# Kernel tuning notes

Measured on AMD Instinct MI355X. Metric: run time of the kernel, lower is better.

## Reference

```python
import jax, jax.numpy as jnp
import numpy as np

B, S, D = 2, 1024, 2048
H, KVH, HD = 16, 4, 128
HID, E, K = 4096, 8, 2
EPS = 1e-5
NEG = -1e9  # finite stand-in for -inf in the causal mask


def setup_inputs() -> dict:
    key = jax.random.key(0)
    ks = jax.random.split(key, 16)
    sc = 0.02
    x = jax.random.normal(ks[0], (B, S, D), jnp.float32)
    # rotary tables (theta = 10000), as cos/sin instead of complex
    inv_freq = 1.0 / (10000.0 ** (jnp.arange(0, HD, 2, dtype=jnp.float32) / HD))
    t = jnp.arange(S, dtype=jnp.float32)
    fr = jnp.outer(t, inv_freq)  # [S, HD/2]
    freqs_cos, freqs_sin = jnp.cos(fr), jnp.sin(fr)
    positions = jnp.arange(S, dtype=jnp.int32)
    mask = jnp.where(jnp.tril(jnp.ones((S, S), bool)), 0.0, NEG).astype(jnp.float32)
    attn_norm_w = jnp.ones((D,), jnp.float32)
    ffn_norm_w = jnp.ones((D,), jnp.float32)
    wq = jax.random.normal(ks[1], (D, H * HD), jnp.float32) * sc
    wk = jax.random.normal(ks[2], (D, KVH * HD), jnp.float32) * sc
    wv = jax.random.normal(ks[3], (D, KVH * HD), jnp.float32) * sc
    wo = jax.random.normal(ks[4], (H * HD, D), jnp.float32) * sc
    gate_w = jax.random.normal(ks[5], (D, E), jnp.float32) * sc
    w1 = jax.random.normal(ks[6], (E, D, HID), jnp.float32) * sc
    w2 = jax.random.normal(ks[7], (E, HID, D), jnp.float32) * sc
    w3 = jax.random.normal(ks[8], (E, D, HID), jnp.float32) * sc
    return dict(x=x, freqs_cos=freqs_cos, freqs_sin=freqs_sin, positions=positions,
                mask=mask, attn_norm_w=attn_norm_w, ffn_norm_w=ffn_norm_w,
                wq=wq, wk=wk, wv=wv, wo=wo, gate_w=gate_w, w1=w1, w2=w2, w3=w3)


def rmsnorm(x, w):
    xf = x.astype(jnp.float32)
    n = xf * jax.lax.rsqrt(jnp.mean(xf * xf, axis=-1, keepdims=True) + EPS)
    return n.astype(x.dtype) * w


def rope(t, cos, sin):
    # t: [B,S,nh,HD]; interleaved (real, imag) pairs like torch.view_as_complex
    tr = t.reshape(*t.shape[:-1], HD // 2, 2)
    xr, xi = tr[..., 0], tr[..., 1]
    c = cos[None, :, None, :]
    s = sin[None, :, None, :]
    out = jnp.stack([xr * c - xi * s, xr * s + xi * c], axis=-1)
    return out.reshape(t.shape)


def block_fwd(x, freqs_cos, freqs_sin, mask, attn_norm_w, ffn_norm_w,
              wq, wk, wv, wo, gate_w, w1, w2, w3):
    # ---- attention ----
    h = rmsnorm(x, attn_norm_w)
    q = (h @ wq).reshape(B, S, H, HD)
    k = (h @ wk).reshape(B, S, KVH, HD)
    v = (h @ wv).reshape(B, S, KVH, HD)
    q = rope(q, freqs_cos, freqs_sin)
    k = rope(k, freqs_cos, freqs_sin)
    rep = H // KVH
    k = jnp.repeat(k, rep, axis=2)  # [B,S,H,HD]
    v = jnp.repeat(v, rep, axis=2)
    scale = HD ** -0.5
    scores = jnp.einsum('bqhd,bkhd->bhqk', q, k) * scale + mask[None, None]
    probs = jax.nn.softmax(scores.astype(jnp.float32), axis=-1).astype(q.dtype)
    attn = jnp.einsum('bhqk,bkhd->bqhd', probs, v).reshape(B, S, H * HD)
    h1 = x + attn @ wo
    # ---- MoE FFN ----
    t = rmsnorm(h1, ffn_norm_w).reshape(-1, D)  # [T,D]
    logits = t @ gate_w  # [T,E]
    topw, sel = jax.lax.top_k(logits, K)
    topw = jax.nn.softmax(topw.astype(jnp.float32), axis=-1).astype(t.dtype)
    out = jnp.zeros_like(t)
    for i in range(E):
        coef = jnp.sum(jnp.where(sel == i, topw, 0.0), axis=-1, keepdims=True)  # [T,1]
        ff = (jax.nn.silu(t @ w1[i]) * (t @ w3[i])) @ w2[i]
        out = out + coef * ff
    return h1 + out.reshape(B, S, D)


def reference(x, freqs_cos, freqs_sin, positions, mask, attn_norm_w, ffn_norm_w,
              wq, wk, wv, wo, gate_w, w1, w2, w3):
    # prefill branch (positions.shape[0] > 1): KV-cache scatter is a write-only
    # side effect in the original and does not affect this output.
    del positions
    return block_fwd(x, freqs_cos, freqs_sin, mask, attn_norm_w, ffn_norm_w,
                     wq, wk, wv, wo, gate_w, w1, w2, w3)
```

## Files before the change

kernel.cpp:

```cpp
#include <hip/hip_runtime.h>

typedef unsigned short u16;
typedef unsigned int u32;
typedef __bf16 bf16x8 __attribute__((ext_vector_type(8)));
typedef _Float16 f16;
typedef f16 f16x8 __attribute__((ext_vector_type(8)));
typedef float f32x4 __attribute__((ext_vector_type(4)));
typedef u32 u32x2 __attribute__((ext_vector_type(2)));

#define DEVFN __device__ __forceinline__

constexpr int kB = 2, kS = 1024, kD = 2048, kH = 16, kKVH = 4, kHD = 128;
constexpr int kHID = 4096, kE = 8;
constexpr int kRows = kB * kS;
constexpr int kQKVN = kH*kHD + 2*kKVH*kHD;
constexpr int kSlotsPad = 5120;
constexpr int kMaxTiles = 40;
constexpr float kEps = 1e-5f;
constexpr float kNeg = -1000000000.0f;
constexpr float kScale = 0.08838834764831845f;

DEVFN u16 f2bf(float f) {
  u32 u = __float_as_uint(f);
  return (u16)((u + 0x7fffu + ((u >> 16) & 1u)) >> 16);
}
DEVFN float bf2f(u16 u) { u32 v = ((u32)u) << 16; return __uint_as_float(v); }

DEVFN void split8v(float4 a, float4 b, f16x8& hi, f16x8& lo) {
  float v[8] = {a.x, a.y, a.z, a.w, b.x, b.y, b.z, b.w};
  #pragma unroll
  for (int e = 0; e < 8; ++e) {
    f16 h = (f16)v[e];
    hi[e] = h;
    lo[e] = (f16)(v[e] - (float)h);
  }
}

DEVFN void gll16(const void* g, void* l) {
  __builtin_amdgcn_global_load_lds(
      (const __attribute__((address_space(1))) void*)g,
      (__attribute__((address_space(3))) void*)l, 16, 0, 0);
}

DEVFN u32x2 pk4bf(float a, float b, float c, float d) {
  union { __bf16 h[4]; u32x2 w; } u;
  u.h[0] = (__bf16)a; u.h[1] = (__bf16)b;
  u.h[2] = (__bf16)c; u.h[3] = (__bf16)d;
  return u.w;
}

__global__ __launch_bounds__(256) void rms_split_kernel(const float* __restrict__ in,
    const float* __restrict__ w, f16* __restrict__ oh, f16* __restrict__ ol) {
  int row = blockIdx.x, tid = threadIdx.x;
  const float* x = in + (size_t)row * kD;
  float4 v0 = *(const float4*)&x[tid*8];
  float4 v1 = *(const float4*)&x[tid*8+4];
  float ss = v0.x*v0.x+v0.y*v0.y+v0.z*v0.z+v0.w*v0.w
           + v1.x*v1.x+v1.y*v1.y+v1.z*v1.z+v1.w*v1.w;
  #pragma unroll
  for (int off = 32; off; off >>= 1) ss += __shfl_xor(ss, off);
  __shared__ float red[4];
  if ((tid & 63) == 0) red[tid >> 6] = ss;
  __syncthreads();
  float tot = red[0] + red[1] + red[2] + red[3];
  float rs = rsqrtf(tot * (1.0f/kD) + kEps);
  float4 w0 = *(const float4*)&w[tid*8];
  float4 w1 = *(const float4*)&w[tid*8+4];
  float4 o0, o1;
  o0.x = v0.x*rs*w0.x; o0.y = v0.y*rs*w0.y; o0.z = v0.z*rs*w0.z; o0.w = v0.w*rs*w0.w;
  o1.x = v1.x*rs*w1.x; o1.y = v1.y*rs*w1.y; o1.z = v1.z*rs*w1.z; o1.w = v1.w*rs*w1.w;
  f16x8 hi, lo;
  split8v(o0, o1, hi, lo);
  *(f16x8*)&oh[(size_t)row*kD + tid*8] = hi;
  *(f16x8*)&ol[(size_t)row*kD + tid*8] = lo;
}

__global__ __launch_bounds__(256) void rms_bf16_kernel(const float* __restrict__ in,
    const float* __restrict__ w, u16* __restrict__ out) {
  int row = blockIdx.x, tid = threadIdx.x;
  const float* x = in + (size_t)row * kD;
  float4 v0 = *(const float4*)&x[tid*8];
  float4 v1 = *(const float4*)&x[tid*8+4];
  float ss = v0.x*v0.x+v0.y*v0.y+v0.z*v0.z+v0.w*v0.w
           + v1.x*v1.x+v1.y*v1.y+v1.z*v1.z+v1.w*v1.w;
  #pragma unroll
  for (int off = 32; off; off >>= 1) ss += __shfl_xor(ss, off);
  __shared__ float red[4];
  if ((tid & 63) == 0) red[tid >> 6] = ss;
  __syncthreads();
  float tot = red[0] + red[1] + red[2] + red[3];
  float rs = rsqrtf(tot * (1.0f/kD) + kEps);
  float4 w0 = *(const float4*)&w[tid*8];
  float4 w1 = *(const float4*)&w[tid*8+4];
  union { int4 i4; u16 u[8]; } pk;
  pk.u[0] = f2bf(v0.x*rs*w0.x); pk.u[1] = f2bf(v0.y*rs*w0.y);
  pk.u[2] = f2bf(v0.z*rs*w0.z); pk.u[3] = f2bf(v0.w*rs*w0.w);
  pk.u[4] = f2bf(v1.x*rs*w1.x); pk.u[5] = f2bf(v1.y*rs*w1.y);
  pk.u[6] = f2bf(v1.z*rs*w1.z); pk.u[7] = f2bf(v1.w*rs*w1.w);
  *(int4*)&out[(size_t)row*kD + tid*8] = pk.i4;
}

__global__ void transpose_split_kernel(const float* __restrict__ in,
    f16* __restrict__ hi, f16* __restrict__ lo, int R, int C, int noff, int ldout) {
  __shared__ float tile[32][33];
  int c0 = blockIdx.x * 32, r0 = blockIdx.y * 32;
  int tx = threadIdx.x, ty = threadIdx.y;
  #pragma unroll
  for (int i = 0; i < 32; i += 8)
    tile[ty + i][tx] = in[(size_t)(r0 + ty + i) * C + c0 + tx];
  __syncthreads();
  #pragma unroll
  for (int i = 0; i < 32; i += 8) {
    float v = tile[tx][ty + i];
    f16 h = (f16)v;
    size_t o = (size_t)(noff + c0 + ty + i) * ldout + r0 + tx;
    hi[o] = h;
    lo[o] = (f16)(v - (float)h);
  }
}

__global__ void vt_split_kernel(const float* __restrict__ qkv,
    f16* __restrict__ vTh, f16* __restrict__ vTl) {
  __shared__ float tile[32][33];
  int s0 = blockIdx.x * 32, c0 = blockIdx.y * 32, b = blockIdx.z;
  int tx = threadIdx.x, ty = threadIdx.y;
  #pragma unroll
  for (int i = 0; i < 32; i += 8)
    tile[ty + i][tx] = qkv[(size_t)(b*kS + s0 + ty + i) * kQKVN + kH*kHD + kKVH*kHD + c0 + tx];
  __syncthreads();
  #pragma unroll
  for (int i = 0; i < 32; i += 8) {
    float v = tile[tx][ty + i];
    f16 h = (f16)v;
    size_t o = (size_t)(b*kKVH*kHD + c0 + ty + i) * kS + s0 + tx;
    vTh[o] = h;
    vTl[o] = (f16)(v - (float)h);
  }
}

template<bool ADDX>
__global__ __launch_bounds__(256) void gemm_sf16_kernel(
    const f16* __restrict__ Ah0, const f16* __restrict__ Al0, int lda,
    const f16* __restrict__ Bh0, const f16* __restrict__ Bl0,
    float* __restrict__ C, int ldc, int coff,
    const float* __restrict__ X, int ldx, int K) {
  __shared__ __align__(16) u16 Ah[128*64], Al[128*64], Bh[128*64], Bl[128*64];
  int tid = threadIdx.x, lane = tid & 63, w = tid >> 6;
  int bm = blockIdx.y * 128, bn = blockIdx.x * 128;
  int wr = w >> 1, wc = w & 1;
  int hg = lane >> 4, lid = lane & 15;
  f32x4 acc[4][4] = {};
  const f16 *aH[4], *aL[4], *bH[4], *bL[4];
  #pragma unroll
  for (int j = 0; j < 4; ++j) {
    int r = w*32 + j*8 + (lane >> 3);
    int colc = ((lane & 7) ^ (r & 7)) * 8;
    aH[j] = Ah0 + (size_t)(bm + r) * lda + colc;
    aL[j] = Al0 + (size_t)(bm + r) * lda + colc;
    bH[j] = Bh0 + (size_t)(bn + r) * K + colc;
    bL[j] = Bl0 + (size_t)(bn + r) * K + colc;
  }
  const char* AhB = (const char*)Ah; const char* AlB = (const char*)Al;
  const char* BhB = (const char*)Bh; const char* BlB = (const char*)Bl;
  for (int kt = 0; kt < K; kt += 64) {
    __syncthreads();
    #pragma unroll
    for (int j = 0; j < 4; ++j) {
      int lb = w*2048 + j*512;
      gll16(aH[j] + kt, &Ah[lb]);
      gll16(aL[j] + kt, &Al[lb]);
      gll16(bH[j] + kt, &Bh[lb]);
      gll16(bL[j] + kt, &Bl[lb]);
    }
    __syncthreads();
    #pragma unroll
    for (int kk = 0; kk < 2; ++kk) {
      f16x8 ah[4], al[4], bh[4], bl[4];
      #pragma unroll
      for (int f = 0; f < 4; ++f) {
        int rA = wr*64 + f*16 + lid;
        int oA = (rA*128 + kk*64 + hg*16) ^ ((rA & 7) << 4);
        ah[f] = *(const f16x8*)(AhB + oA);
        al[f] = *(const f16x8*)(AlB + oA);
        int rB = wc*64 + f*16 + lid;
        int oB = (rB*128 + kk*64 + hg*16) ^ ((rB & 7) << 4);
        bh[f] = *(const f16x8*)(BhB + oB);
        bl[f] = *(const f16x8*)(BlB + oB);
      }
      __builtin_amdgcn_s_setprio(1);
      #pragma unroll
      for (int i = 0; i < 4; ++i)
        #pragma unroll
        for (int j = 0; j < 4; ++j) {
          acc[i][j] = __builtin_amdgcn_mfma_f32_16x16x32_f16(ah[i], bh[j], acc[i][j], 0, 0, 0);
          acc[i][j] = __builtin_amdgcn_mfma_f32_16x16x32_f16(ah[i], bl[j], acc[i][j], 0, 0, 0);
          acc[i][j] = __builtin_amdgcn_mfma_f32_16x16x32_f16(al[i], bh[j], acc[i][j], 0, 0, 0);
        }
      __builtin_amdgcn_s_setprio(0);
    }
  }
  #pragma unroll
  for (int i = 0; i < 4; ++i) {
    #pragma unroll
    for (int rr = 0; rr < 4; ++rr) {
      size_t gr = (size_t)(bm + wr*64 + i*16 + hg*4 + rr);
      #pragma unroll
      for (int j = 0; j < 4; ++j) {
        int gc = bn + wc*64 + j*16 + lid;
        float v = acc[i][j][rr];
        if (ADDX) v += X[gr * ldx + gc];
        C[gr * ldc + coff + gc] = v;
      }
    }
  }
}

__global__ __launch_bounds__(256) void rope_kernel(float* __restrict__ qkv,
    const float* __restrict__ fc, const float* __restrict__ fs,
    f16* __restrict__ Kh, f16* __restrict__ Kl) {
  int idx = blockIdx.x * 256 + threadIdx.x;
  constexpr int NQ = kB*kS*kH*(kHD/2);
  constexpr int NK = kB*kS*kKVH*(kHD/2);
  if (idx < NQ) {
    int i = idx & 63, h = (idx >> 6) & 15, s = (idx >> 10) & 1023, b = idx >> 20;
    size_t base = ((size_t)(b*kS + s))*kQKVN + h*kHD + 2*i;
    float c = fc[s*64 + i], sn = fs[s*64 + i];
    float xr = qkv[base], xi = qkv[base+1];
    qkv[base]   = xr*c - xi*sn;
    qkv[base+1] = xr*sn + xi*c;
  } else {
    int j = idx - NQ; if (j >= NK) return;
    int i = j & 63, h = (j >> 6) & 3, s = (j >> 8) & 1023, b = j >> 18;
    size_t src = ((size_t)(b*kS + s))*kQKVN + kH*kHD + h*kHD + 2*i;
    float c = fc[s*64 + i], sn = fs[s*64 + i];
    float xr = qkv[src], xi = qkv[src+1];
    float o0 = xr*c - xi*sn, o1 = xr*sn + xi*c;
    size_t dst = (((size_t)(b*kKVH + h))*kS + s)*kHD + 2*i;
    f16 h0 = (f16)o0, h1 = (f16)o1;
    Kh[dst]   = h0; Kl[dst]   = (f16)(o0 - (float)h0);
    Kh[dst+1] = h1; Kl[dst+1] = (f16)(o1 - (float)h1);
  }
}

__global__ __launch_bounds__(256) void attn_sf16_kernel(const float* __restrict__ qkv,
    const f16* __restrict__ Ksh, const f16* __restrict__ Ksl,
    const f16* __restrict__ vTh, const f16* __restrict__ vTl,
    f16* __restrict__ outh, f16* __restrict__ outl) {
  int qt = (int)gridDim.x - 1 - blockIdx.x;
  int h = blockIdx.y, b = blockIdx.z;
  int kvh = h >> 2;
  int q0 = qt * 64;
  __shared__ __align__(16) char Kh[64*128*2], Kl[64*128*2];
  __shared__ __align__(16) char Vh[128*64*2], Vl[128*64*2];
  __shared__ __align__(16) char Ph[4][16*64*2], Pl[4][16*64*2];
  int tid = threadIdx.x, lane = tid & 63, w = tid >> 6;
  int hg = lane >> 4, lid = lane & 15;

  f16x8 qh[4], ql[4];
  {
    const float* qrow = qkv + (size_t)(b*kS + q0 + w*16 + lid) * kQKVN + h*kHD;
    #pragma unroll
    for (int ks = 0; ks < 4; ++ks) {
      float4 a = *(const float4*)(qrow + ks*32 + hg*8);
      float4 c = *(const float4*)(qrow + ks*32 + hg*8 + 4);
      split8v(a, c, qh[ks], ql[ks]);
    }
  }
  f32x4 oacc[8] = {};
  float m[4] = {-3.0e38f, -3.0e38f, -3.0e38f, -3.0e38f};
  float lsum[4] = {};
  char* Phw = Ph[w];
  char* Plw = Pl[w];

  for (int kt = 0; kt <= qt; ++kt) {
    __syncthreads();
    {
      int r = tid >> 2, c0 = (tid & 3) * 32;
      const f16* khr = Ksh + ((size_t)(b*kKVH + kvh)*kS + kt*64 + r) * kHD + c0;
      const f16* klr = Ksl + ((size_t)(b*kKVH + kvh)*kS + kt*64 + r) * kHD + c0;
      #pragma unroll
      for (int s8 = 0; s8 < 4; ++s8) {
        int4 hi = *(const int4*)(khr + s8*8);
        int4 lo = *(const int4*)(klr + s8*8);
        int off = (r*256 + c0*2 + s8*16) ^ ((r & 7) << 4);
        *(int4*)(Kh + off) = hi;
        *(int4*)(Kl + off) = lo;
      }
    }
    {
      int r = tid >> 1, c0 = (tid & 1) * 32;
      const f16* vhr = vTh + (size_t)(b*kKVH*kHD + kvh*kHD + r) * kS + kt*64 + c0;
      const f16* vlr = vTl + (size_t)(b*kKVH*kHD + kvh*kHD + r) * kS + kt*64 + c0;
      #pragma unroll
      for (int s8 = 0; s8 < 4; ++s8) {
        int4 hi = *(const int4*)(vhr + s8*8);
        int4 lo = *(const int4*)(vlr + s8*8);
        int off = (r*128 + c0*2 + s8*16) ^ ((r & 7) << 4);
        *(int4*)(Vh + off) = hi;
        *(int4*)(Vl + off) = lo;
      }
    }
    __syncthreads();

    f32x4 sacc[4] = {};
    __builtin_amdgcn_s_setprio(1);
    #pragma unroll
    for (int ks = 0; ks < 4; ++ks) {
      #pragma unroll
      for (int j = 0; j < 4; ++j) {
        int rB = j*16 + lid;
        int off = (rB*256 + ks*64 + hg*16) ^ ((rB & 7) << 4);
        f16x8 kh = *(const f16x8*)(Kh + off);
        f16x8 klo = *(const f16x8*)(Kl + off);
        sacc[j] = __builtin_amdgcn_mfma_f32_16x16x32_f16(qh[ks], kh, sacc[j], 0, 0, 0);
        sacc[j] = __builtin_amdgcn_mfma_f32_16x16x32_f16(qh[ks], klo, sacc[j], 0, 0, 0);
        sacc[j] = __builtin_amdgcn_mfma_f32_16x16x32_f16(ql[ks], kh, sacc[j], 0, 0, 0);
      }
    }
    __builtin_amdgcn_s_setprio(0);
    float s[4][4], ps[4][4];
    bool diag = (kt == qt);
    #pragma unroll
    for (int j = 0; j < 4; ++j)
      #pragma unroll
      for (int r = 0; r < 4; ++r) {
        float v = sacc[j][r] * kScale;
        if (diag) {
          int kvabs = kt*64 + j*16 + lid;
          int qabs = q0 + w*16 + hg*4 + r;
          if (kvabs > qabs) v = kNeg;
        }
        s[j][r] = v;
      }
    float pm[4], cf[4];
    #pragma unroll
    for (int r = 0; r < 4; ++r) {
      pm[r] = fmaxf(fmaxf(s[0][r], s[1][r]), fmaxf(s[2][r], s[3][r]));
      #pragma unroll
      for (int msk = 1; msk < 16; msk <<= 1) pm[r] = fmaxf(pm[r], __shfl_xor(pm[r], msk));
      float mn = fmaxf(m[r], pm[r]);
      cf[r] = __expf(m[r] - mn);
      m[r] = mn;
    }
    #pragma unroll
    for (int j2 = 0; j2 < 8; ++j2)
      #pragma unroll
      for (int r = 0; r < 4; ++r) oacc[j2][r] *= cf[r];
    float rs[4] = {};
    #pragma unroll
    for (int j = 0; j < 4; ++j)
      #pragma unroll
      for (int r = 0; r < 4; ++r) {
        float p = __expf(s[j][r] - m[r]);
        ps[j][r] = p;
        rs[r] += p;
      }
    #pragma unroll
    for (int r = 0; r < 4; ++r) lsum[r] = lsum[r]*cf[r] + rs[r];
    #pragma unroll
    for (int j = 0; j < 4; ++j)
      #pragma unroll
      for (int r = 0; r < 4; ++r) {
        int q = hg*4 + r;
        int off = (q*128 + (j*16 + lid)*2) ^ ((q & 7) << 4);
        f16 ph = (f16)ps[j][r];
        *(f16*)(Phw + off) = ph;
        *(f16*)(Plw + off) = (f16)(ps[j][r] - (float)ph);
      }
    #pragma unroll
    for (int kk2 = 0; kk2 < 2; ++kk2) {
      int oP = (lid*128 + kk2*64 + hg*16) ^ ((lid & 7) << 4);
      f16x8 pa_h = *(const f16x8*)(Phw + oP);
      f16x8 pa_l = *(const f16x8*)(Plw + oP);
      __builtin_amdgcn_s_setprio(1);
      #pragma unroll
      for (int j2 = 0; j2 < 8; ++j2) {
        int rV = j2*16 + lid;
        int off = (rV*128 + kk2*64 + hg*16) ^ ((rV & 7) << 4);
        f16x8 vh = *(const f16x8*)(Vh + off);
        f16x8 vl = *(const f16x8*)(Vl + off);
        oacc[j2] = __builtin_amdgcn_mfma_f32_16x16x32_f16(pa_h, vh, oacc[j2], 0, 0, 0);
        oacc[j2] = __builtin_amdgcn_mfma_f32_16x16x32_f16(pa_h, vl, oacc[j2], 0, 0, 0);
        oacc[j2] = __builtin_amdgcn_mfma_f32_16x16x32_f16(pa_l, vh, oacc[j2], 0, 0, 0);
      }
      __builtin_amdgcn_s_setprio(0);
    }
  }
  #pragma unroll
  for (int r = 0; r < 4; ++r) {
    #pragma unroll
    for (int msk = 1; msk < 16; msk <<= 1) lsum[r] += __shfl_xor(lsum[r], msk);
    lsum[r] = 1.f / lsum[r];
  }
  #pragma unroll
  for (int j2 = 0; j2 < 8; ++j2)
    #pragma unroll
    for (int r = 0; r < 4; ++r) {
      size_t o = (size_t)(b*kS + q0 + w*16 + hg*4 + r) * kD + h*kHD + j2*16 + lid;
      float v = oacc[j2][r] * lsum[r];
      f16 hh = (f16)v;
      outh[o] = hh;
      outl[o] = (f16)(v - (float)hh);
    }
}

__global__ void zero_counts_kernel(int* counts) {
  if (threadIdx.x < kE) counts[threadIdx.x] = 0;
}

__global__ __launch_bounds__(64) void gate_kernel(const float* __restrict__ h1,
    const float* __restrict__ wn, const float* __restrict__ gw,
    int* __restrict__ packA, int* __restrict__ packB,
    float* __restrict__ cA, float* __restrict__ cB,
    int* __restrict__ lists, int* __restrict__ counts) {
  int row = blockIdx.x, lane = threadIdx.x;
  const float* x = h1 + (size_t)row * kD;
  float ss = 0.f;
  for (int d = lane; d < kD; d += 64) { float v = x[d]; ss = fmaf(v, v, ss); }
  #pragma unroll
  for (int off = 32; off; off >>= 1) ss += __shfl_xor(ss, off);
  float rs = rsqrtf(ss * (1.0f/kD) + kEps);
  float acc[kE] = {};
  for (int d = lane; d < kD; d += 64) {
    float g = x[d] * rs * wn[d];
    const float* gr = gw + (size_t)d * kE;
    #pragma unroll
    for (int e = 0; e < kE; ++e) acc[e] = fmaf(g, gr[e], acc[e]);
  }
  #pragma unroll
  for (int e = 0; e < kE; ++e)
    #pragma unroll
    for (int off = 32; off; off >>= 1) acc[e] += __shfl_xor(acc[e], off);
  if (lane == 0) {
    int i1 = 0; float l1 = acc[0];
    #pragma unroll
    for (int e = 1; e < kE; ++e) if (acc[e] > l1) { l1 = acc[e]; i1 = e; }
    int i2 = -1; float l2 = -3.4e38f;
    #pragma unroll
    for (int e = 0; e < kE; ++e) if (e != i1 && acc[e] > l2) { l2 = acc[e]; i2 = e; }
    float e2 = __expf(l2 - l1);
    float inv = 1.f / (1.f + e2);
    int p1 = atomicAdd(&counts[i1], 1); lists[i1*kRows + p1] = row;
    int p2 = atomicAdd(&counts[i2], 1); lists[i2*kRows + p2] = row;
    packA[row] = i1*2048 + p1; cA[row] = inv;
    packB[row] = i2*2048 + p2; cB[row] = e2 * inv;
  }
}

__global__ void prefix_kernel(const int* __restrict__ counts,
    int* __restrict__ padbase, int* __restrict__ tileTab) {
  if (threadIdx.x == 0) {
    int base = 0, idx = 0;
    for (int e = 0; e < kE; ++e) {
      padbase[e] = base;
      int nt = (counts[e] + 127) >> 7;
      for (int t = 0; t < nt; ++t) tileTab[idx++] = (e << 8) | t;
      base += nt << 7;
    }
    for (; idx < kMaxTiles; ++idx) tileTab[idx] = -1;
  }
}

__global__ __launch_bounds__(512, 4) void gemm_up_kernel(
    const u16* __restrict__ A, const float* __restrict__ W1, const float* __restrict__ W3,
    u16* __restrict__ hid, const int* __restrict__ lists,
    const int* __restrict__ counts, const int* __restrict__ padbase,
    const int* __restrict__ tileTab) {
  int tab = tileTab[blockIdx.y];
  if (tab < 0) return;
  int e = tab >> 8, mb = tab & 255;
  int cnt = counts[e];
  int bm = mb * 128;
  int slot0 = padbase[e] + bm;
  const int* ids = lists + e * kRows;
  int g = blockIdx.x;
  __shared__ __align__(16) char SM[65536];
  u16* As[2]   = { (u16*)SM, (u16*)(SM + 16384) };
  char* B1s[2] = { SM + 32768, SM + 40960 };
  char* B3s[2] = { SM + 49152, SM + 57344 };
  int tid = threadIdx.x, lane = tid & 63, w = tid >> 6;
  int wr = w >> 2, wcc = w & 3;
  int hg = lane >> 4, lid = lane & 15;
  f32x4 acc[4][2] = {};

  const u16* aP[2];
  #pragma unroll
  for (int j = 0; j < 2; ++j) {
    int r = w*16 + j*8 + (lane >> 3);
    int colc = ((lane & 7) ^ (r & 7)) * 8;
    int rr = bm + r; if (rr >= cnt) rr = cnt - 1;
    aP[j] = A + (size_t)ids[rr] * kD + colc;
  }
  const float* b1e = W1 + (size_t)e*kD*kHID + (size_t)g*64 + lane;
  const float* b3e = W3 + (size_t)e*kD*kHID + (size_t)g*64 + lane;
  int wOff[2];
  #pragma unroll
  for (int s = 0; s < 2; ++s)
    wOff[s] = (lane*128 + w*16 + s*8) ^ ((lane & 7) << 4);

  auto stageA = [&](int buf, int t) {
    int kt = t * 64;
    #pragma unroll
    for (int j = 0; j < 2; ++j) gll16(aP[j] + kt, &As[buf][w*1024 + j*512]);
  };
  float r1v[2][4], r3v[2][4];
  auto loadB = [&](int t) {
    int kt = t * 64;
    #pragma unroll
    for (int s = 0; s < 2; ++s)
      #pragma unroll
      for (int j = 0; j < 4; ++j) {
        size_t ko = (size_t)(kt + w*8 + s*4 + j) * kHID;
        r1v[s][j] = b1e[ko];
        r3v[s][j] = b3e[ko];
      }
  };
  auto writeB = [&](int buf) {
    #pragma unroll
    for (int s = 0; s < 2; ++s) {
      *(u32x2*)(B1s[buf] + wOff[s]) = pk4bf(r1v[s][0], r1v[s][1], r1v[s][2], r1v[s][3]);
      *(u32x2*)(B3s[buf] + wOff[s]) = pk4bf(r3v[s][0], r3v[s][1], r3v[s][2], r3v[s][3]);
    }
  };
  auto compute = [&](int buf) {
    const char* AsB = (const char*)As[buf];
    const char* Bb = (wcc >= 2) ? B3s[buf] : B1s[buf];
    #pragma unroll
    for (int kk = 0; kk < 2; ++kk) {
      bf16x8 af[4], bfv[2];
      #pragma unroll
      for (int f = 0; f < 4; ++f) {
        int rA = wr*64 + f*16 + lid;
        af[f] = *(const bf16x8*)(AsB + ((rA*128 + kk*64 + hg*16) ^ ((rA & 7) << 4)));
      }
      #pragma unroll
      for (int f = 0; f < 2; ++f) {
        int rB = (wcc & 1)*32 + f*16 + lid;
        bfv[f] = *(const bf16x8*)(Bb + ((rB*128 + kk*64 + hg*16) ^ ((rB & 7) << 4)));
      }
      __builtin_amdgcn_s_setprio(1);
      #pragma unroll
      for (int i = 0; i < 4; ++i)
        #pragma unroll
        for (int j = 0; j < 2; ++j)
          acc[i][j] = __builtin_amdgcn_mfma_f32_16x16x32_bf16(af[i], bfv[j], acc[i][j], 0, 0, 0);
      __builtin_amdgcn_s_setprio(0);
    }
  };

  constexpr int NT = kD / 64;
  stageA(0, 0);
  loadB(0);
  writeB(0);
  __syncthreads();
  for (int t = 0; t < NT; t += 2) {
    stageA(1, t+1); loadB(t+1);
    compute(0);
    writeB(1);
    __syncthreads();
    if (t+2 < NT) { stageA(0, t+2); loadB(t+2); }
    compute(1);
    if (t+2 < NT) writeB(0);
    __syncthreads();
  }

  float* Xch = (float*)SM;
  if (wcc < 2) {
    #pragma unroll
    for (int i = 0; i < 4; ++i)
      #pragma unroll
      for (int rr = 0; rr < 4; ++rr) {
        int row = wr*64 + i*16 + hg*4 + rr;
        #pragma unroll
        for (int j = 0; j < 2; ++j)
          Xch[row*64 + (wcc & 1)*32 + j*16 + lid] = acc[i][j][rr];
      }
  }
  __syncthreads();
  if (wcc >= 2) {
    #pragma unroll
    for (int i = 0; i < 4; ++i)
      #pragma unroll
      for (int rr = 0; rr < 4; ++rr) {
        int row = wr*64 + i*16 + hg*4 + rr;
        int gr = bm + row;
        if (gr >= cnt) continue;
        u16* orow = hid + (size_t)(slot0 + row) * kHID + g*64 + (wcc & 1)*32;
        #pragma unroll
        for (int j = 0; j < 2; ++j) {
          int col = j*16 + lid;
          float g1 = Xch[row*64 + (wcc & 1)*32 + col];
          float g3 = acc[i][j][rr];
          orow[col] = f2bf(g1 / (1.f + __expf(-g1)) * g3);
        }
      }
  }
}

__global__ __launch_bounds__(512, 4) void gemm_down_kernel(
    const u16* __restrict__ hid, const float* __restrict__ W2,
    u16* __restrict__ ff, const int* __restrict__ padbase,
    const int* __restrict__ tileTab) {
  int tab = tileTab[blockIdx.y];
  if (tab < 0) return;
  int e = tab >> 8, mb = tab & 255;
  int slot0 = padbase[e] + mb * 128;
  int bn = blockIdx.x * 128;
  __shared__ __align__(16) char SM[65536];
  u16* As[2] = { (u16*)SM, (u16*)(SM + 16384) };
  char* Bs[2] = { SM + 32768, SM + 49152 };
  int tid = threadIdx.x, lane = tid & 63, w = tid >> 6;
  int wr = w >> 2, wc = w & 3;
  int hg = lane >> 4, lid = lane & 15;
  f32x4 acc[4][2] = {};

  const u16* aP[2];
  #pragma unroll
  for (int j = 0; j < 2; ++j) {
    int r = w*16 + j*8 + (lane >> 3);
    int colc = ((lane & 7) ^ (r & 7)) * 8;
    aP[j] = hid + (size_t)(slot0 + r) * kHID + colc;
  }
  int nrow = tid & 127;
  int kq = tid >> 7;
  const float* b2e = W2 + (size_t)e*kHID*kD + (size_t)bn + nrow;
  int wOff[4];
  #pragma unroll
  for (int s = 0; s < 4; ++s)
    wOff[s] = (nrow*128 + kq*32 + s*8) ^ ((nrow & 7) << 4);

  auto stageA = [&](int buf, int t) {
    int kt = t * 64;
    #pragma unroll
    for (int j = 0; j < 2; ++j) gll16(aP[j] + kt, &As[buf][w*1024 + j*512]);
  };
  float rbv[4][4];
  auto loadB = [&](int t) {
    int kt = t * 64;
    #pragma unroll
    for (int s = 0; s < 4; ++s)
      #pragma unroll
      for (int j = 0; j < 4; ++j)
        rbv[s][j] = b2e[(size_t)(kt + kq*16 + s*4 + j) * kD];
  };
  auto writeB = [&](int buf) {
    #pragma unroll
    for (int s = 0; s < 4; ++s)
      *(u32x2*)(Bs[buf] + wOff[s]) = pk4bf(rbv[s][0], rbv[s][1], rbv[s][2], rbv[s][3]);
  };
  auto compute = [&](int buf) {
    const char* AsB = (const char*)As[buf];
    const char* Bb = Bs[buf];
    #pragma unroll
    for (int kk = 0; kk < 2; ++kk) {
      bf16x8 af[4], bfv[2];
      #pragma unroll
      for (int f = 0; f < 4; ++f) {
        int rA = wr*64 + f*16 + lid;
        af[f] = *(const bf16x8*)(AsB + ((rA*128 + kk*64 + hg*16) ^ ((rA & 7) << 4)));
      }
      #pragma unroll
      for (int f = 0; f < 2; ++f) {
        int rB = wc*32 + f*16 + lid;
        bfv[f] = *(const bf16x8*)(Bb + ((rB*128 + kk*64 + hg*16) ^ ((rB & 7) << 4)));
      }
      __builtin_amdgcn_s_setprio(1);
      #pragma unroll
      for (int i = 0; i < 4; ++i)
        #pragma unroll
        for (int j = 0; j < 2; ++j)
          acc[i][j] = __builtin_amdgcn_mfma_f32_16x16x32_bf16(af[i], bfv[j], acc[i][j], 0, 0, 0);
      __builtin_amdgcn_s_setprio(0);
    }
  };

  constexpr int NT = kHID / 64;
  stageA(0, 0);
  loadB(0);
  writeB(0);
  __syncthreads();
  for (int t = 0; t < NT; t += 2) {
    stageA(1, t+1); loadB(t+1);
    compute(0);
    writeB(1);
    __syncthreads();
    if (t+2 < NT) { stageA(0, t+2); loadB(t+2); }
    compute(1);
    if (t+2 < NT) writeB(0);
    __syncthreads();
  }

  #pragma unroll
  for (int i = 0; i < 4; ++i)
    #pragma unroll
    for (int rr = 0; rr < 4; ++rr) {
      int row = wr*64 + i*16 + hg*4 + rr;
      u16* orow = ff + (size_t)(slot0 + row) * kD + bn;
      #pragma unroll
      for (int j = 0; j < 2; ++j)
        orow[wc*32 + j*16 + lid] = f2bf(acc[i][j][rr]);
    }
}

__global__ __launch_bounds__(256) void moe_combine_kernel(
    const u16* __restrict__ ff, const int* __restrict__ padbase,
    const int* __restrict__ packA, const int* __restrict__ packB,
    const float* __restrict__ cA, const float* __restrict__ cB,
    float* __restrict__ outp) {
  int row = blockIdx.x, tid = threadIdx.x;
  int pa = packA[row], pb = packB[row];
  int sa = padbase[pa >> 11] + (pa & 2047);
  int sb = padbase[pb >> 11] + (pb & 2047);
  float ca = cA[row], cb = cB[row];
  union { int4 i4; u16 u[8]; } va, vb;
  va.i4 = *(const int4*)(ff + (size_t)sa * kD + tid*8);
  vb.i4 = *(const int4*)(ff + (size_t)sb * kD + tid*8);
  float* o = outp + (size_t)row * kD + tid*8;
  float4 o0 = *(const float4*)o;
  float4 o1 = *(const float4*)(o + 4);
  o0.x += ca*bf2f(va.u[0]) + cb*bf2f(vb.u[0]);
  o0.y += ca*bf2f(va.u[1]) + cb*bf2f(vb.u[1]);
  o0.z += ca*bf2f(va.u[2]) + cb*bf2f(vb.u[2]);
  o0.w += ca*bf2f(va.u[3]) + cb*bf2f(vb.u[3]);
  o1.x += ca*bf2f(va.u[4]) + cb*bf2f(vb.u[4]);
  o1.y += ca*bf2f(va.u[5]) + cb*bf2f(vb.u[5]);
  o1.z += ca*bf2f(va.u[6]) + cb*bf2f(vb.u[6]);
  o1.w += ca*bf2f(va.u[7]) + cb*bf2f(vb.u[7]);
  *(float4*)o = o0;
  *(float4*)(o + 4) = o1;
}

extern "C" void kernel_launch(void* const* d_in, const int* in_sizes, int n_in,
                              void* d_out, int out_size, void* d_ws, size_t ws_size,
                              hipStream_t stream) {
  const float* x    = (const float*)d_in[0];
  const float* fcos = (const float*)d_in[1];
  const float* fsin = (const float*)d_in[2];
  const float* anw  = (const float*)d_in[5];
  const float* fnw  = (const float*)d_in[6];
  const float* wq   = (const float*)d_in[7];
  const float* wk   = (const float*)d_in[8];
  const float* wv   = (const float*)d_in[9];
  const float* wo   = (const float*)d_in[10];
  const float* gw   = (const float*)d_in[11];
  const float* w1   = (const float*)d_in[12];
  const float* w2   = (const float*)d_in[13];
  const float* w3   = (const float*)d_in[14];
  float* outp = (float*)d_out;

  char* ws = (char*)d_ws;
  size_t off = 0;
  auto alloc = [&](size_t bytes) -> void* {
    void* p = ws + off; off += (bytes + 255) & ~(size_t)255; return p;
  };
  f16* h16h   = (f16*)alloc((size_t)kRows*kD*2);
  f16* h16l   = (f16*)alloc((size_t)kRows*kD*2);
  float* qkv  = (float*)alloc((size_t)kRows*kQKVN*4);
  f16* Ksh    = (f16*)alloc((size_t)kB*kKVH*kS*kHD*2);
  f16* Ksl    = (f16*)alloc((size_t)kB*kKVH*kS*kHD*2);
  f16* vTh    = (f16*)alloc((size_t)kB*kKVH*kHD*kS*2);
  f16* vTl    = (f16*)alloc((size_t)kB*kKVH*kHD*kS*2);
  f16* a16h   = (f16*)alloc((size_t)kRows*kD*2);
  f16* a16l   = (f16*)alloc((size_t)kRows*kD*2);
  u16* tbf    = (u16*)alloc((size_t)kRows*kD*2);
  int* packA  = (int*)alloc(kRows*4);
  int* packB  = (int*)alloc(kRows*4);
  float* cAv  = (float*)alloc(kRows*4);
  float* cBv  = (float*)alloc(kRows*4);
  int* counts = (int*)alloc(kE*4);
  int* padbase= (int*)alloc(kE*4);
  int* tileTab= (int*)alloc(kMaxTiles*4);
  int* lists  = (int*)alloc((size_t)kE*kRows*4);
  f16* Bqh    = (f16*)alloc((size_t)kQKVN*kD*2);
  f16* Bql    = (f16*)alloc((size_t)kQKVN*kD*2);
  f16* Bwh    = (f16*)alloc((size_t)kD*kD*2);
  f16* Bwl    = (f16*)alloc((size_t)kD*kD*2);
  u16* hid    = (u16*)alloc((size_t)kSlotsPad*kHID*2);
  u16* ffb    = (u16*)alloc((size_t)kSlotsPad*kD*2);

  transpose_split_kernel<<<dim3(kD/32, kD/32), dim3(32,8), 0, stream>>>(wq, Bqh, Bql, kD, 2048, 0, kD);
  transpose_split_kernel<<<dim3(512/32, kD/32), dim3(32,8), 0, stream>>>(wk, Bqh, Bql, kD, 512, 2048, kD);
  transpose_split_kernel<<<dim3(512/32, kD/32), dim3(32,8), 0, stream>>>(wv, Bqh, Bql, kD, 512, 2560, kD);
  transpose_split_kernel<<<dim3(kD/32, kD/32), dim3(32,8), 0, stream>>>(wo, Bwh, Bwl, kD, kD, 0, kD);

  rms_split_kernel<<<kRows, 256, 0, stream>>>(x, anw, h16h, h16l);
  gemm_sf16_kernel<false><<<dim3(kQKVN/128, kRows/128), 256, 0, stream>>>(
      h16h, h16l, kD, Bqh, Bql, qkv, kQKVN, 0, nullptr, 0, kD);
  rope_kernel<<<(kB*kS*(kH+kKVH)*(kHD/2))/256, 256, 0, stream>>>(qkv, fcos, fsin, Ksh, Ksl);
  vt_split_kernel<<<dim3(kS/32, (kKVH*kHD)/32, kB), dim3(32,8), 0, stream>>>(qkv, vTh, vTl);
  attn_sf16_kernel<<<dim3(kS/64, kH, kB), 256, 0, stream>>>(qkv, Ksh, Ksl, vTh, vTl, a16h, a16l);
  gemm_sf16_kernel<true><<<dim3(kD/128, kRows/128), 256, 0, stream>>>(
      a16h, a16l, kD, Bwh, Bwl, outp, kD, 0, x, kD, kD);

  zero_counts_kernel<<<1, 64, 0, stream>>>(counts);
  gate_kernel<<<kRows, 64, 0, stream>>>(outp, fnw, gw, packA, packB, cAv, cBv, lists, counts);
  prefix_kernel<<<1, 64, 0, stream>>>(counts, padbase, tileTab);
  rms_bf16_kernel<<<kRows, 256, 0, stream>>>(outp, fnw, tbf);

  gemm_up_kernel<<<dim3(kHID/64, kMaxTiles), 512, 0, stream>>>(
      tbf, w1, w3, hid, lists, counts, padbase, tileTab);
  gemm_down_kernel<<<dim3(kD/128, kMaxTiles), 512, 0, stream>>>(
      hid, w2, ffb, padbase, tileTab);
  moe_combine_kernel<<<kRows, 256, 0, stream>>>(
      ffb, padbase, packA, packB, cAv, cBv, outp);
}
```

Baseline: 864.0 us.

## Deepen MoE GEMM pipeline with two in-flight B register sets and partial waitcnt barriers

Restructures the up and down MoE GEMM main loops so the global loads of the fp32 weight tiles run two k-steps ahead, using two register buffers (even and odd). The plain __syncthreads are replaced with explicit barriers that wait on lgkmcnt and a partial vmcnt(18), so the async LDS loads of A can stay in flight across a barrier. Launch-bound minimum occupancy is dropped to allow more registers. This targets exposed global-load latency, at the cost of higher register pressure and fragile hand-counted vmcnt values.

```diff
diff --git a/kernel.cpp b/kernel.cpp
--- a/kernel.cpp
+++ b/kernel.cpp
@@ -48,6 +48,22 @@
   u.h[2] = (__bf16)c; u.h[3] = (__bf16)d;
   return u.w;
 }
+
+DEVFN void baronly() { __builtin_amdgcn_sched_barrier(0);
+  __builtin_amdgcn_s_barrier();
+  __builtin_amdgcn_sched_barrier(0); }
+DEVFN void barlgkm() { __builtin_amdgcn_sched_barrier(0);
+  asm volatile("s_waitcnt lgkmcnt(0)" ::: "memory");
+  __builtin_amdgcn_s_barrier();
+  __builtin_amdgcn_sched_barrier(0); }
+DEVFN void barvm18() { __builtin_amdgcn_sched_barrier(0);
+  asm volatile("s_waitcnt vmcnt(18) lgkmcnt(0)" ::: "memory");
+  __builtin_amdgcn_s_barrier();
+  __builtin_amdgcn_sched_barrier(0); }
+DEVFN void barvm0() { __builtin_amdgcn_sched_barrier(0);
+  asm volatile("s_waitcnt vmcnt(0) lgkmcnt(0)" ::: "memory");
+  __builtin_amdgcn_s_barrier();
+  __builtin_amdgcn_sched_barrier(0); }
 
 __global__ __launch_bounds__(256) void rms_split_kernel(const float* __restrict__ in,
     const float* __restrict__ w, f16* __restrict__ oh, f16* __restrict__ ol) {
@@ -461,7 +477,7 @@
   }
 }
 
-__global__ __launch_bounds__(512, 4) void gemm_up_kernel(
+__global__ __launch_bounds__(512) void gemm_up_kernel(
     const u16* __restrict__ A, const float* __restrict__ W1, const float* __restrict__ W3,
     u16* __restrict__ hid, const int* __restrict__ lists,
     const int* __restrict__ counts, const int* __restrict__ padbase,
@@ -503,23 +519,22 @@
     #pragma unroll
     for (int j = 0; j < 2; ++j) gll16(aP[j] + kt, &As[buf][w*1024 + j*512]);
   };
-  float r1v[2][4], r3v[2][4];
-  auto loadB = [&](int t) {
+  auto loadB = [&](float r1[2][4], float r3[2][4], int t) {
     int kt = t * 64;
     #pragma unroll
     for (int s = 0; s < 2; ++s)
       #pragma unroll
       for (int j = 0; j < 4; ++j) {
         size_t ko = (size_t)(kt + w*8 + s*4 + j) * kHID;
-        r1v[s][j] = b1e[ko];
-        r3v[s][j] = b3e[ko];
+        r1[s][j] = b1e[ko];
+        r3[s][j] = b3e[ko];
       }
   };
-  auto writeB = [&](int buf) {
+  auto writeB = [&](int buf, float r1[2][4], float r3[2][4]) {
     #pragma unroll
     for (int s = 0; s < 2; ++s) {
-      *(u32x2*)(B1s[buf] + wOff[s]) = pk4bf(r1v[s][0], r1v[s][1], r1v[s][2], r1v[s][3]);
-      *(u32x2*)(B3s[buf] + wOff[s]) = pk4bf(r3v[s][0], r3v[s][1], r3v[s][2], r3v[s][3]);
+      *(u32x2*)(B1s[buf] + wOff[s]) = pk4bf(r1[s][0], r1[s][1], r1[s][2], r1[s][3]);
+      *(u32x2*)(B3s[buf] + wOff[s]) = pk4bf(r3[s][0], r3[s][1], r3[s][2], r3[s][3]);
     }
   };
   auto compute = [&](int buf) {
@@ -548,21 +563,33 @@
     }
   };
 
+  float r1E[2][4], r3E[2][4], r1O[2][4], r3O[2][4];
   constexpr int NT = kD / 64;
-  stageA(0, 0);
-  loadB(0);
-  writeB(0);
+  stageA(0, 0); stageA(1, 1);
+  loadB(r1E, r3E, 0);
+  loadB(r1O, r3O, 1);
+  writeB(0, r1E, r3E);
+  barlgkm();
+  for (int t = 0; t + 2 < NT; t += 2) {
+    loadB(r1E, r3E, t+2);
+    compute(0);
+    baronly();
+    stageA(0, t+2);
+    writeB(1, r1O, r3O);
+    barvm18();
+    loadB(r1O, r3O, t+3);
+    compute(1);
+    baronly();
+    stageA(1, t+3);
+    writeB(0, r1E, r3E);
+    barvm18();
+  }
+  compute(0);
+  baronly();
+  writeB(1, r1O, r3O);
+  barvm0();
+  compute(1);
   __syncthreads();
-  for (int t = 0; t < NT; t += 2) {
-    stageA(1, t+1); loadB(t+1);
-    compute(0);
-    writeB(1);
-    __syncthreads();
-    if (t+2 < NT) { stageA(0, t+2); loadB(t+2); }
-    compute(1);
-    if (t+2 < NT) writeB(0);
-    __syncthreads();
-  }
 
   float* Xch = (float*)SM;
   if (wcc < 2) {
@@ -597,7 +624,7 @@
   }
 }
 
-__global__ __launch_bounds__(512, 4) void gemm_down_kernel(
+__global__ __launch_bounds__(512) void gemm_down_kernel(
     const u16* __restrict__ hid, const float* __restrict__ W2,
     u16* __restrict__ ff, const int* __restrict__ padbase,
     const int* __restrict__ tileTab) {
@@ -634,19 +661,18 @@
     #pragma unroll
     for (int j = 0; j < 2; ++j) gll16(aP[j] + kt, &As[buf][w*1024 + j*512]);
   };
-  float rbv[4][4];
-  auto loadB = [&](int t) {
+  auto loadB = [&](float r[4][4], int t) {
     int kt = t * 64;
     #pragma unroll
     for (int s = 0; s < 4; ++s)
       #pragma unroll
       for (int j = 0; j < 4; ++j)
-        rbv[s][j] = b2e[(size_t)(kt + kq*16 + s*4 + j) * kD];
+        r[s][j] = b2e[(size_t)(kt + kq*16 + s*4 + j) * kD];
   };
-  auto writeB = [&](int buf) {
+  auto writeB = [&](int buf, float r[4][4]) {
     #pragma unroll
     for (int s = 0; s < 4; ++s)
-      *(u32x2*)(Bs[buf] + wOff[s]) = pk4bf(rbv[s][0], rbv[s][1], rbv[s][2], rbv[s][3]);
+      *(u32x2*)(Bs[buf] + wOff[s]) = pk4bf(r[s][0], r[s][1], r[s][2], r[s][3]);
   };
   auto compute = [&](int buf) {
     const char* AsB = (const char*)As[buf];
@@ -674,21 +700,33 @@
     }
   };
 
+  float rE[4][4], rO[4][4];
   constexpr int NT = kHID / 64;
-  stageA(0, 0);
-  loadB(0);
-  writeB(0);
+  stageA(0, 0); stageA(1, 1);
+  loadB(rE, 0);
+  loadB(rO, 1);
+  writeB(0, rE);
+  barlgkm();
+  for (int t = 0; t + 2 < NT; t += 2) {
+    loadB(rE, t+2);
+    compute(0);
+    baronly();
+    stageA(0, t+2);
+    writeB(1, rO);
+    barvm18();
+    loadB(rO, t+3);
+    compute(1);
+    baronly();
+    stageA(1, t+3);
+    writeB(0, rE);
+    barvm18();
+  }
+  compute(0);
+  baronly();
+  writeB(1, rO);
+  barvm0();
+  compute(1);
   __syncthreads();
-  for (int t = 0; t < NT; t += 2) {
-    stageA(1, t+1); loadB(t+1);
-    compute(0);
-    writeB(1);
-    __syncthreads();
-    if (t+2 < NT) { stageA(0, t+2); loadB(t+2); }
-    compute(1);
-    if (t+2 < NT) writeB(0);
-    __syncthreads();
-  }
 
   #pragma unroll
   for (int i = 0; i < 4; ++i)
```

Result: slower. 927.1 us (+7.3%).
